# Optimization experiments

Hardware: AMD Instinct MI355X
Metric: run time of the kernel (lower is better)

Reference implementation:

```python
import jax, jax.numpy as jnp
import numpy as np
import math

B, S, DIM = 2, 2048, 2048
H, KVH, HD = 32, 8, 64          # n_heads, n_kv_heads, head_dim = dim // n_heads
N_REP = H // KVH                # 4
ROPE_THETA = 10000.0


def _apply_rotary(x, cos, sin):
    # x: [B, S, nh, HD]; cos/sin: [S, HD//2]
    # pairs (x[..., 2i], x[..., 2i+1]) treated as complex a+ib, multiplied by cos+isin
    xr = x.reshape(*x.shape[:-1], HD // 2, 2)
    a, b = xr[..., 0], xr[..., 1]
    c = cos[None, :, None, :]
    s = sin[None, :, None, :]
    out = jnp.stack([a * c - b * s, a * s + b * c], axis=-1)
    return out.reshape(x.shape)


def setup_inputs() -> dict:
    key = jax.random.key(0)
    ks = jax.random.split(key, 5)
    x = jax.random.normal(ks[0], (B, S, DIM), dtype=jnp.float32)
    scale = 1.0 / math.sqrt(DIM)
    wq = jax.random.normal(ks[1], (DIM, H * HD), dtype=jnp.float32) * scale
    wk = jax.random.normal(ks[2], (DIM, KVH * HD), dtype=jnp.float32) * scale
    wv = jax.random.normal(ks[3], (DIM, KVH * HD), dtype=jnp.float32) * scale
    wo = jax.random.normal(ks[4], (H * HD, DIM), dtype=jnp.float32) * scale
    # RoPE frequencies: freqs_cis = exp(i * t * theta^{-2k/HD}), k = 0..HD/2-1
    inv_freq = 1.0 / (ROPE_THETA ** (jnp.arange(0, HD, 2, dtype=jnp.float32) / HD))
    angles = jnp.arange(S, dtype=jnp.float32)[:, None] * inv_freq[None, :]  # [S, HD//2]
    freqs_cos = jnp.cos(angles)
    freqs_sin = jnp.sin(angles)
    # causal mask: True = masked out
    mask = jnp.triu(jnp.ones((1, 1, S, S), dtype=bool), k=1)
    return {"x": x, "wq": wq, "wk": wk, "wv": wv, "wo": wo,
            "freqs_cos": freqs_cos, "freqs_sin": freqs_sin,
            "mask": mask, "start_pos": 0}


def reference(x, wq, wk, wv, wo, freqs_cos, freqs_sin, mask, start_pos):
    del start_pos  # unused, matching original
    bsz, seqlen, _ = x.shape
    xq = (x @ wq).reshape(bsz, seqlen, H, HD)
    xk = (x @ wk).reshape(bsz, seqlen, KVH, HD)
    xv = (x @ wv).reshape(bsz, seqlen, KVH, HD)
    xq = _apply_rotary(xq, freqs_cos, freqs_sin)
    xk = _apply_rotary(xk, freqs_cos, freqs_sin)
    # repeat_kv: [B,S,KVH,HD] -> [B,S,H,HD]
    xk = jnp.repeat(xk[:, :, :, None, :], N_REP, axis=3).reshape(bsz, seqlen, H, HD)
    xv = jnp.repeat(xv[:, :, :, None, :], N_REP, axis=3).reshape(bsz, seqlen, H, HD)
    xq = jnp.transpose(xq, (0, 2, 1, 3))  # [B,H,S,HD]
    xk = jnp.transpose(xk, (0, 2, 1, 3))
    xv = jnp.transpose(xv, (0, 2, 1, 3))
    scores = jnp.einsum('bhqd,bhkd->bhqk', xq, xk) / math.sqrt(HD)
    scores = jnp.where(mask, -jnp.inf, scores)
    probs = jax.nn.softmax(scores.astype(jnp.float32), axis=-1).astype(xq.dtype)
    out = jnp.einsum('bhqk,bhkd->bhqd', probs, xv)
    out = jnp.transpose(out, (0, 2, 1, 3)).reshape(bsz, seqlen, H * HD)
    return out @ wo
```

## Files before the change

### kernel.cpp

```cpp
#include <hip/hip_runtime.h>


using u16   = unsigned short;
using u32   = unsigned int;
using f32x4 = __attribute__((ext_vector_type(4))) float;
using f32x16= __attribute__((ext_vector_type(16))) float;
using s16x8 = __attribute__((ext_vector_type(8))) short;
using b16x8 = __attribute__((ext_vector_type(8))) __bf16;
using u16x4 = __attribute__((ext_vector_type(4))) unsigned short;
using u32x4 = __attribute__((ext_vector_type(4))) u32;

__device__ __forceinline__ u16 f2bf(float f) {
  u32 u = __builtin_bit_cast(u32, f);
  u = (u + 0x7fffu + ((u >> 16) & 1u)) >> 16;
  return (u16)u;
}
__device__ __forceinline__ float bf2f(u32 lo16) {
  return __builtin_bit_cast(float, lo16 << 16);
}

__device__ __forceinline__ f32x4 mfma16(s16x8 a, s16x8 b, f32x4 c) {
  return __builtin_amdgcn_mfma_f32_16x16x32_bf16(
      __builtin_bit_cast(b16x8, a), __builtin_bit_cast(b16x8, b), c, 0, 0, 0);
}
__device__ __forceinline__ f32x16 mfma32(s16x8 a, s16x8 b, f32x16 c) {
  return __builtin_amdgcn_mfma_f32_32x32x16_bf16(
      __builtin_bit_cast(b16x8, a), __builtin_bit_cast(b16x8, b), c, 0, 0, 0);
}

__device__ __forceinline__ void gload_lds16(const void* g, void* l) {
  __builtin_amdgcn_global_load_lds(
      (const __attribute__((address_space(1))) void*)g,
      (__attribute__((address_space(3))) void*)l, 16, 0, 0);
}

__device__ __forceinline__ u32 cvtpk(float lo, float hi) {
  u32 r; asm("v_cvt_pk_bf16_f32 %0, %1, %2" : "=v"(r) : "v"(lo), "v"(hi));
  return r;
}

__device__ __forceinline__ float fexp2(float x) {
#if __has_builtin(__builtin_amdgcn_exp2f)
  return __builtin_amdgcn_exp2f(x);
#else
  return exp2f(x);
#endif
}

__global__ __launch_bounds__(256) void cvt_kernel(const float* __restrict__ src,
                                                  u16* __restrict__ dst, int n4) {
  int i = blockIdx.x * 256 + threadIdx.x;
  if (i >= n4) return;
  f32x4 v = *(const f32x4*)(src + (size_t)i * 4);
  u16x4 r;
#pragma unroll
  for (int j = 0; j < 4; ++j) r[j] = f2bf(v[j]);
  *(u16x4*)(dst + (size_t)i * 4) = r;
}

__global__ __launch_bounds__(256) void tcvt_kernel(const float* __restrict__ src,
                                                   u16* __restrict__ dst, int N) {
  __shared__ float t[32][33];
  const int n0 = blockIdx.x * 32, k0 = blockIdx.y * 32;
  const int tx = threadIdx.x & 31, ty = threadIdx.x >> 5;
#pragma unroll
  for (int r = 0; r < 4; ++r)
    t[ty + 8 * r][tx] = src[(size_t)(k0 + ty + 8 * r) * N + n0 + tx];
  __syncthreads();
#pragma unroll
  for (int r = 0; r < 4; ++r)
    dst[(size_t)(n0 + ty + 8 * r) * 2048 + k0 + tx] = f2bf(t[tx][ty + 8 * r]);
}

__global__ __launch_bounds__(256) void rope_kernel(u16* __restrict__ qkv,
                                                   const float* __restrict__ cs,
                                                   const float* __restrict__ sn) {
  const int m = blockIdx.x;
  const int p = blockIdx.y * 256 + threadIdx.x;
  const int s = m & 2047;
  int col, d2;
  if (p < 1024) { col = 2 * p; d2 = p & 31; }
  else { int pk = p - 1024; col = 2048 + 2 * pk; d2 = pk & 31; }
  const float c = cs[s * 32 + d2], si = sn[s * 32 + d2];
  u32* addr = (u32*)&qkv[(size_t)m * 3072 + col];
  u32 v = *addr;
  float a = bf2f(v & 0xffffu), b = bf2f(v >> 16);
  float na = a * c - b * si;
  float nb = a * si + b * c;
  *addr = (u32)f2bf(na) | ((u32)f2bf(nb) << 16);
}

__global__ __launch_bounds__(256) void vt_kernel(const u16* __restrict__ qkv,
                                                 u16* __restrict__ VtG) {
  __shared__ u16 t[64][65];
  const int s0 = blockIdx.x * 64;
  const int bk = blockIdx.y;
  const int b = bk >> 3, kvh = bk & 7;
  const int tx = threadIdx.x & 63, ty = threadIdx.x >> 6;
#pragma unroll
  for (int r = 0; r < 16; ++r)
    t[ty + 4 * r][tx] =
        qkv[(size_t)(b * 2048 + s0 + ty + 4 * r) * 3072 + 2560 + kvh * 64 + tx];
  __syncthreads();
#pragma unroll
  for (int r = 0; r < 16; ++r)
    VtG[(size_t)(bk * 64 + ty + 4 * r) * 2048 + s0 + tx] = t[tx][ty + 4 * r];
}

template <bool BF16OUT>
__global__ __launch_bounds__(256) void gemm_bt(const u16* __restrict__ A,
                                               const u16* __restrict__ Bt,
                                               void* __restrict__ Cv,
                                               int M, int N, int K, int GX) {
  __shared__ u16 As[2][128 * 32];
  __shared__ u16 Bs[2][128 * 32];
  const int tid = threadIdx.x;
  const int wid = tid >> 6, lane = tid & 63;
  const int l15 = lane & 15, lq = lane >> 4;
  const int wr = wid >> 1, wc = wid & 1;
  const int cpx = gridDim.x >> 3;
  const int swz = (blockIdx.x & 7) * cpx + (blockIdx.x >> 3);
  const int m0 = (swz / GX) * 128, n0 = (swz % GX) * 128;

  const int srow16 = lane >> 2;
  const int k8 = (lane & 3) * 8;

  auto STAGE = [&](int bb, int kt) {
#pragma unroll
    for (int i = 0; i < 2; ++i) {
      const int r = wid * 2 + i;
      const int row = r * 16 + srow16;
      gload_lds16(A + (size_t)(m0 + row) * K + kt + k8, &As[bb][r * 512]);
      gload_lds16(Bt + (size_t)(n0 + row) * K + kt + k8, &Bs[bb][r * 512]);
    }
  };

  f32x4 acc[4][4] = {};
  STAGE(0, 0);
  __syncthreads();
  int cur = 0;
  for (int kt = 0; kt < K; kt += 32) {
    if (kt + 32 < K) STAGE(cur ^ 1, kt + 32);
    s16x8 af[4], bf[4];
#pragma unroll
    for (int i = 0; i < 4; ++i)
      af[i] = *(const s16x8*)&As[cur][(wr * 64 + i * 16 + l15) * 32 + 8 * lq];
#pragma unroll
    for (int j = 0; j < 4; ++j)
      bf[j] = *(const s16x8*)&Bs[cur][(wc * 64 + j * 16 + l15) * 32 + 8 * lq];
#pragma unroll
    for (int i = 0; i < 4; ++i)
#pragma unroll
      for (int j = 0; j < 4; ++j)
        acc[i][j] = mfma16(af[i], bf[j], acc[i][j]);
    __syncthreads();
    cur ^= 1;
  }

  u16* Cb = (u16*)Cv;
  float* Cf = (float*)Cv;
#pragma unroll
  for (int i = 0; i < 4; ++i)
#pragma unroll
    for (int j = 0; j < 4; ++j)
#pragma unroll
      for (int r = 0; r < 4; ++r) {
        const int row = m0 + wr * 64 + i * 16 + 4 * lq + r;
        const int col = n0 + wc * 64 + j * 16 + l15;
        if constexpr (BF16OUT) Cb[(size_t)row * N + col] = f2bf(acc[i][j][r]);
        else                   Cf[(size_t)row * N + col] = acc[i][j][r];
      }
}

__global__ __launch_bounds__(512, 4) void attn_kernel(const u16* __restrict__ qkv,
                                                      const u16* __restrict__ VtG,
                                                      u16* __restrict__ aout) {
  constexpr int QSTR = 3072;
  constexpr float SCL = 0.18033688011112042f;
  const int bx = blockIdx.x;
  const int bh = blockIdx.y;
  const int b = bh >> 5, h = bh & 31, kvh = h >> 2;
  const int tid = threadIdx.x;
  const int w = tid >> 6, g = w >> 2, wq = w & 3;
  const int l31 = tid & 31, hh = (tid >> 5) & 1;

  __shared__ u16 KV[2][2][2][4096];
  __shared__ float cml[256];

  const int u = tid & 255;
  const int srow = u >> 3, sslot = u & 7;
  const int sd8 = (sslot ^ (srow & 7)) * 8;
  const u16* kg = qkv + (size_t)(b * 2048 + srow) * QSTR + 2048 + kvh * 64 + sd8;
  const u16* vg = VtG + (size_t)((b * 8 + kvh) * 64 + srow) * 2048 + sd8;
  const int wg = u >> 6;
  const int xsw = l31 & 7;

  auto STAGE = [&](int buf, int t) {
    const size_t ko = (size_t)t * 64 * QSTR;
    const size_t vo = (size_t)t * 64;
    gload_lds16(kg + ko, &KV[g][0][buf][wg * 512]);
    gload_lds16(kg + ko + (size_t)32 * QSTR, &KV[g][0][buf][2048 + wg * 512]);
    gload_lds16(vg + vo, &KV[g][1][buf][wg * 512]);
    gload_lds16(vg + vo + (size_t)32 * 2048, &KV[g][1][buf][2048 + wg * 512]);
  };

  float* cO = (float*)&KV[1][0][0][0];

  auto process = [&](int qt) {
    const int h1 = qt + 1;
    const int q_abs = qt * 128 + wq * 32 + l31;
    const u16* qrow = qkv + (size_t)(b * 2048 + q_abs) * QSTR + h * 64;
    s16x8 qf[4];
#pragma unroll
    for (int s = 0; s < 4; ++s) qf[s] = *(const s16x8*)(qrow + 16 * s + 8 * hh);

    f32x16 o0 = {}, o1 = {};
    float mrun = 0.f, lrun = 0.f;

    STAGE(0, g * h1);
    __syncthreads();

    for (int s = 0; s < h1; ++s) {
      if (s + 1 < h1) STAGE((s + 1) & 1, g * h1 + s + 1);
      const int kv0 = (g * h1 + s) * 64;
      const u16* Kb = &KV[g][0][s & 1][0];
      const u16* Vb = &KV[g][1][s & 1][0];

      f32x16 a0 = {}, a1 = {};
      __builtin_amdgcn_s_setprio(1);
#pragma unroll
      for (int s4 = 0; s4 < 4; ++s4) {
        const int cc = ((2 * s4 + hh) ^ xsw) * 8;
        s16x8 k0 = *(const s16x8*)(Kb + l31 * 64 + cc);
        s16x8 k1 = *(const s16x8*)(Kb + (32 + l31) * 64 + cc);
        a0 = mfma32(k0, qf[s4], a0);
        a1 = mfma32(k1, qf[s4], a1);
      }
      __builtin_amdgcn_s_setprio(0);

      if (kv0 + 63 > qt * 128 + wq * 32) {
#pragma unroll
        for (int r = 0; r < 16; ++r) {
          const int kva = kv0 + (r & 3) + 8 * (r >> 2) + 4 * hh;
          if (kva > q_abs) a0[r] = -3e38f;
          if (kva + 32 > q_abs) a1[r] = -3e38f;
        }
      }

      float mxr = -3e38f;
#pragma unroll
      for (int r = 0; r < 16; ++r) mxr = fmaxf(mxr, fmaxf(a0[r], a1[r]));
      float mx = fmaxf(mxr * SCL, __shfl_xor(mxr * SCL, 32));
      const bool need = __any(mx > mrun + 8.f);
      float mnew = mrun, c1 = 1.f;
      if (need) {
        mnew = fmaxf(mrun, mx);
        c1 = fexp2(mrun - mnew);
      }

      float sum = 0.f;
#pragma unroll
      for (int r = 0; r < 16; ++r) {
        a0[r] = fexp2(__builtin_fmaf(a0[r], SCL, -mnew));
        a1[r] = fexp2(__builtin_fmaf(a1[r], SCL, -mnew));
        sum += a0[r] + a1[r];
      }
      sum += __shfl_xor(sum, 32);
      lrun = lrun * c1 + sum;
      mrun = mnew;
      if (need) {
#pragma unroll
        for (int r = 0; r < 16; ++r) { o0[r] *= c1; o1[r] *= c1; }
      }

      s16x8 pf[4];
#pragma unroll
      for (int s4 = 0; s4 < 4; ++s4) {
        const f32x16& ps = (s4 & 2) ? a1 : a0;
        const int g4 = (s4 & 1) * 8;
        u32 x  = cvtpk(ps[g4 + 0], ps[g4 + 1]);
        u32 x2 = cvtpk(ps[g4 + 2], ps[g4 + 3]);
        u32 y  = cvtpk(ps[g4 + 4], ps[g4 + 5]);
        u32 y2 = cvtpk(ps[g4 + 6], ps[g4 + 7]);
        asm("v_permlane32_swap_b32 %0, %1" : "+v"(x), "+v"(y));
        asm("v_permlane32_swap_b32 %0, %1" : "+v"(x2), "+v"(y2));
        u32x4 fr = {x, x2, y, y2};
        pf[s4] = __builtin_bit_cast(s16x8, fr);
      }

      __builtin_amdgcn_s_setprio(1);
#pragma unroll
      for (int s4 = 0; s4 < 4; ++s4) {
        const int cc = ((2 * s4 + hh) ^ xsw) * 8;
        s16x8 v0f = *(const s16x8*)(Vb + l31 * 64 + cc);
        s16x8 v1f = *(const s16x8*)(Vb + (32 + l31) * 64 + cc);
        o0 = mfma32(v0f, pf[s4], o0);
        o1 = mfma32(v1f, pf[s4], o1);
      }
      __builtin_amdgcn_s_setprio(0);
      __syncthreads();
    }

    const int idx = wq * 32 + l31;
    if (g == 1) {
#pragma unroll
      for (int r = 0; r < 16; ++r) {
        cO[(hh * 16 + r) * 128 + idx] = o0[r];
        cO[(32 + hh * 16 + r) * 128 + idx] = o1[r];
      }
      if (hh == 0) {
        cml[idx] = mrun;
        cml[128 + idx] = lrun;
      }
    }
    __syncthreads();
    if (g == 0) {
      const float mB = cml[idx], lB = cml[128 + idx];
      const float mn = fmaxf(mrun, mB);
      const float sA = fexp2(mrun - mn), sB = fexp2(mB - mn);
      const float inv = 1.f / (lrun * sA + lB * sB);
      u16* ob = aout + (size_t)(b * 2048 + q_abs) * 2048 + h * 64;
#pragma unroll
      for (int gg = 0; gg < 4; ++gg) {
        u16x4 w0, w1;
#pragma unroll
        for (int j = 0; j < 4; ++j) {
          const int r = 4 * gg + j;
          w0[j] = f2bf((o0[r] * sA + cO[(hh * 16 + r) * 128 + idx] * sB) * inv);
          w1[j] = f2bf((o1[r] * sA + cO[(32 + hh * 16 + r) * 128 + idx] * sB) * inv);
        }
        *(u16x4*)(ob + 8 * gg + 4 * hh) = w0;
        *(u16x4*)(ob + 32 + 8 * gg + 4 * hh) = w1;
      }
    }
    __syncthreads();
  };

  process(15 - bx);
  process(bx);
}

extern "C" void kernel_launch(void* const* d_in, const int* in_sizes, int n_in,
                              void* d_out, int out_size, void* d_ws, size_t ws_size,
                              hipStream_t stream) {
  const float* x    = (const float*)d_in[0];
  const float* wq   = (const float*)d_in[1];
  const float* wk   = (const float*)d_in[2];
  const float* wv   = (const float*)d_in[3];
  const float* wo   = (const float*)d_in[4];
  const float* cosT = (const float*)d_in[5];
  const float* sinT = (const float*)d_in[6];
  float* out = (float*)d_out;

  const size_t SZ_XB   = (size_t)4096 * 2048 * 2;
  const size_t SZ_WQKV = (size_t)3072 * 2048 * 2;
  const size_t SZ_WO   = (size_t)2048 * 2048 * 2;
  const size_t SZ_QKV  = (size_t)4096 * 3072 * 2;
  const size_t SZ_ATT  = (size_t)4096 * 2048 * 2;
  if (ws_size < SZ_XB + SZ_WQKV + SZ_WO + SZ_QKV + SZ_ATT) return;

  char* p = (char*)d_ws;
  u16* xb    = (u16*)p; p += SZ_XB;
  u16* wqkvT = (u16*)p; p += SZ_WQKV;
  u16* woT   = (u16*)p; p += SZ_WO;
  u16* qkv   = (u16*)p; p += SZ_QKV;
  u16* attn  = (u16*)p; p += SZ_ATT;
  u16* VtG   = xb;

  cvt_kernel<<<8192, 256, 0, stream>>>(x, xb, 2097152);
  tcvt_kernel<<<dim3(64, 64), 256, 0, stream>>>(wq, wqkvT, 2048);
  tcvt_kernel<<<dim3(16, 64), 256, 0, stream>>>(wk, wqkvT + (size_t)2048 * 2048, 512);
  tcvt_kernel<<<dim3(16, 64), 256, 0, stream>>>(wv, wqkvT + (size_t)2560 * 2048, 512);
  tcvt_kernel<<<dim3(64, 64), 256, 0, stream>>>(wo, woT, 2048);

  gemm_bt<true><<<768, 256, 0, stream>>>(xb, wqkvT, qkv, 4096, 3072, 2048, 24);
  rope_kernel<<<dim3(4096, 5), 256, 0, stream>>>(qkv, cosT, sinT);
  vt_kernel<<<dim3(32, 16), 256, 0, stream>>>(qkv, VtG);
  attn_kernel<<<dim3(8, 64), 512, 0, stream>>>(qkv, VtG, attn);
  gemm_bt<false><<<512, 256, 0, stream>>>(attn, woT, out, 4096, 2048, 2048, 16);
}
```

Before: 208.2 us.

## Fuse RoPE and V-transpose into QKV GEMM epilogue

Adds a dedicated QKV GEMM whose epilogue applies rotary embedding to Q and K columns using lane shuffles, and writes V directly in a transposed layout inside the qkv buffer's V region. This removes the separate rope and V-transpose kernels along with their extra passes over qkv. The attention kernel now reads transposed V from the repacked qkv region instead of a separate buffer. The trade-offs are per-element cos/sin loads in the epilogue and a strided transposed V store pattern.

```diff
diff --git a/kernel.cpp b/kernel.cpp
--- a/kernel.cpp
+++ b/kernel.cpp
@@ -72,39 +72,92 @@
     dst[(size_t)(n0 + ty + 8 * r) * 2048 + k0 + tx] = f2bf(t[tx][ty + 8 * r]);
 }
 
-__global__ __launch_bounds__(256) void rope_kernel(u16* __restrict__ qkv,
-                                                   const float* __restrict__ cs,
-                                                   const float* __restrict__ sn) {
-  const int m = blockIdx.x;
-  const int p = blockIdx.y * 256 + threadIdx.x;
-  const int s = m & 2047;
-  int col, d2;
-  if (p < 1024) { col = 2 * p; d2 = p & 31; }
-  else { int pk = p - 1024; col = 2048 + 2 * pk; d2 = pk & 31; }
-  const float c = cs[s * 32 + d2], si = sn[s * 32 + d2];
-  u32* addr = (u32*)&qkv[(size_t)m * 3072 + col];
-  u32 v = *addr;
-  float a = bf2f(v & 0xffffu), b = bf2f(v >> 16);
-  float na = a * c - b * si;
-  float nb = a * si + b * c;
-  *addr = (u32)f2bf(na) | ((u32)f2bf(nb) << 16);
-}
-
-__global__ __launch_bounds__(256) void vt_kernel(const u16* __restrict__ qkv,
-                                                 u16* __restrict__ VtG) {
-  __shared__ u16 t[64][65];
-  const int s0 = blockIdx.x * 64;
-  const int bk = blockIdx.y;
-  const int b = bk >> 3, kvh = bk & 7;
-  const int tx = threadIdx.x & 63, ty = threadIdx.x >> 6;
-#pragma unroll
-  for (int r = 0; r < 16; ++r)
-    t[ty + 4 * r][tx] =
-        qkv[(size_t)(b * 2048 + s0 + ty + 4 * r) * 3072 + 2560 + kvh * 64 + tx];
+__global__ __launch_bounds__(256) void gemm_qkv(const u16* __restrict__ A,
+                                                const u16* __restrict__ Bt,
+                                                u16* __restrict__ C,
+                                                const float* __restrict__ cs,
+                                                const float* __restrict__ sn) {
+  constexpr int K = 2048, GX = 24;
+  __shared__ u16 As[2][128 * 32];
+  __shared__ u16 Bs[2][128 * 32];
+  const int tid = threadIdx.x;
+  const int wid = tid >> 6, lane = tid & 63;
+  const int l15 = lane & 15, lq = lane >> 4;
+  const int wr = wid >> 1, wc = wid & 1;
+  const int cpx = gridDim.x >> 3;
+  const int swz = (blockIdx.x & 7) * cpx + (blockIdx.x >> 3);
+  const int m0 = (swz / GX) * 128, n0 = (swz % GX) * 128;
+
+  const int srow16 = lane >> 2;
+  const int k8 = (lane & 3) * 8;
+
+  auto STAGE = [&](int bb, int kt) {
+#pragma unroll
+    for (int i = 0; i < 2; ++i) {
+      const int r = wid * 2 + i;
+      const int row = r * 16 + srow16;
+      gload_lds16(A + (size_t)(m0 + row) * K + kt + k8, &As[bb][r * 512]);
+      gload_lds16(Bt + (size_t)(n0 + row) * K + kt + k8, &Bs[bb][r * 512]);
+    }
+  };
+
+  f32x4 acc[4][4] = {};
+  STAGE(0, 0);
   __syncthreads();
-#pragma unroll
-  for (int r = 0; r < 16; ++r)
-    VtG[(size_t)(bk * 64 + ty + 4 * r) * 2048 + s0 + tx] = t[tx][ty + 4 * r];
+  int cur = 0;
+  for (int kt = 0; kt < K; kt += 32) {
+    if (kt + 32 < K) STAGE(cur ^ 1, kt + 32);
+    s16x8 af[4], bf[4];
+#pragma unroll
+    for (int i = 0; i < 4; ++i)
+      af[i] = *(const s16x8*)&As[cur][(wr * 64 + i * 16 + l15) * 32 + 8 * lq];
+#pragma unroll
+    for (int j = 0; j < 4; ++j)
+      bf[j] = *(const s16x8*)&Bs[cur][(wc * 64 + j * 16 + l15) * 32 + 8 * lq];
+#pragma unroll
+    for (int i = 0; i < 4; ++i)
+#pragma unroll
+      for (int j = 0; j < 4; ++j)
+        acc[i][j] = mfma16(af[i], bf[j], acc[i][j]);
+    __syncthreads();
+    cur ^= 1;
+  }
+
+  if (n0 < 2560) {
+    const float sgn = (l15 & 1) ? 1.f : -1.f;
+#pragma unroll
+    for (int j = 0; j < 4; ++j) {
+      const int col = n0 + wc * 64 + j * 16 + l15;
+      const int d2 = (col & 63) >> 1;
+#pragma unroll
+      for (int i = 0; i < 4; ++i)
+#pragma unroll
+        for (int r = 0; r < 4; ++r) {
+          const int row = m0 + wr * 64 + i * 16 + 4 * lq + r;
+          const int s = row & 2047;
+          const float c = cs[s * 32 + d2], si = sn[s * 32 + d2];
+          const float v = acc[i][j][r];
+          const float p = __shfl_xor(v, 1);
+          C[(size_t)row * 3072 + col] = f2bf(v * c + sgn * (p * si));
+        }
+    }
+  } else {
+    const int b = m0 >> 11;
+#pragma unroll
+    for (int j = 0; j < 4; ++j) {
+      const int dg = (n0 - 2560) + wc * 64 + j * 16 + l15;
+      const int vr = (b * 8 + (dg >> 6)) * 64 + (dg & 63);
+#pragma unroll
+      for (int i = 0; i < 4; ++i) {
+        const int s0 = (m0 & 2047) + wr * 64 + i * 16 + 4 * lq;
+        u16x4 wv;
+#pragma unroll
+        for (int r = 0; r < 4; ++r) wv[r] = f2bf(acc[i][j][r]);
+        u16* dst = C + (size_t)(vr * 4 + (s0 >> 9)) * 3072 + 2560 + (s0 & 511);
+        *(u16x4*)dst = wv;
+      }
+    }
+  }
 }
 
 template <bool BF16OUT>
@@ -173,7 +226,6 @@
 }
 
 __global__ __launch_bounds__(512, 4) void attn_kernel(const u16* __restrict__ qkv,
-                                                      const u16* __restrict__ VtG,
                                                       u16* __restrict__ aout) {
   constexpr int QSTR = 3072;
   constexpr float SCL = 0.18033688011112042f;
@@ -191,17 +243,17 @@
   const int srow = u >> 3, sslot = u & 7;
   const int sd8 = (sslot ^ (srow & 7)) * 8;
   const u16* kg = qkv + (size_t)(b * 2048 + srow) * QSTR + 2048 + kvh * 64 + sd8;
-  const u16* vg = VtG + (size_t)((b * 8 + kvh) * 64 + srow) * 2048 + sd8;
+  const u16* vg = qkv + (size_t)(((b * 8 + kvh) * 64 + srow) * 4) * QSTR + 2560 + sd8;
   const int wg = u >> 6;
   const int xsw = l31 & 7;
 
   auto STAGE = [&](int buf, int t) {
     const size_t ko = (size_t)t * 64 * QSTR;
-    const size_t vo = (size_t)t * 64;
     gload_lds16(kg + ko, &KV[g][0][buf][wg * 512]);
     gload_lds16(kg + ko + (size_t)32 * QSTR, &KV[g][0][buf][2048 + wg * 512]);
-    gload_lds16(vg + vo, &KV[g][1][buf][wg * 512]);
-    gload_lds16(vg + vo + (size_t)32 * 2048, &KV[g][1][buf][2048 + wg * 512]);
+    const u16* va = vg + (size_t)(t >> 3) * QSTR + (t & 7) * 64;
+    gload_lds16(va, &KV[g][1][buf][wg * 512]);
+    gload_lds16(va + (size_t)128 * QSTR, &KV[g][1][buf][2048 + wg * 512]);
   };
 
   float* cO = (float*)&KV[1][0][0][0];
@@ -365,7 +417,6 @@
   u16* woT   = (u16*)p; p += SZ_WO;
   u16* qkv   = (u16*)p; p += SZ_QKV;
   u16* attn  = (u16*)p; p += SZ_ATT;
-  u16* VtG   = xb;
 
   cvt_kernel<<<8192, 256, 0, stream>>>(x, xb, 2097152);
   tcvt_kernel<<<dim3(64, 64), 256, 0, stream>>>(wq, wqkvT, 2048);
@@ -373,9 +424,7 @@
   tcvt_kernel<<<dim3(16, 64), 256, 0, stream>>>(wv, wqkvT + (size_t)2560 * 2048, 512);
   tcvt_kernel<<<dim3(64, 64), 256, 0, stream>>>(wo, woT, 2048);
 
-  gemm_bt<true><<<768, 256, 0, stream>>>(xb, wqkvT, qkv, 4096, 3072, 2048, 24);
-  rope_kernel<<<dim3(4096, 5), 256, 0, stream>>>(qkv, cosT, sinT);
-  vt_kernel<<<dim3(32, 16), 256, 0, stream>>>(qkv, VtG);
-  attn_kernel<<<dim3(8, 64), 512, 0, stream>>>(qkv, VtG, attn);
+  gemm_qkv<<<768, 256, 0, stream>>>(xb, wqkvT, qkv, cosT, sinT);
+  attn_kernel<<<dim3(8, 64), 512, 0, stream>>>(qkv, attn);
   gemm_bt<false><<<512, 256, 0, stream>>>(attn, woT, out, 4096, 2048, 2048, 16);
 }
```

Result: slower. 224.0 us (+7.6%).
